# Optimization experiments

Hardware: AMD Instinct MI355X
Metric: run time of the kernel (lower is better)

The kernel has to match this reference:

```python
import jax, jax.numpy as jnp
import numpy as np

HIDDEN = 1024
HEADS = 16
HEAD_DIM = HIDDEN // HEADS

def setup_inputs() -> dict:
    key = jax.random.key(0)
    k1, k2, k3 = jax.random.split(key, 3)
    scale = 1.0 / np.sqrt(HIDDEN)
    return {
        "x": jax.random.normal(k1, (2, 2048, HIDDEN), dtype=jnp.float32),
        "w_qkv": jax.random.normal(k2, (HIDDEN, 3 * HIDDEN), dtype=jnp.float32) * scale,
        "b_qkv": jnp.zeros((3 * HIDDEN,), dtype=jnp.float32),
        "w_out": jax.random.normal(k3, (HIDDEN, HIDDEN), dtype=jnp.float32) * scale,
        "b_out": jnp.zeros((HIDDEN,), dtype=jnp.float32),
    }

def reference(x, w_qkv, b_qkv, w_out, b_out):
    B, S, H = x.shape
    qkv = x @ w_qkv + b_qkv                              # (B,S,3H)
    qkv = qkv.reshape(B, S, 3, HEADS, HEAD_DIM)
    qkv = jnp.transpose(qkv, (2, 0, 3, 1, 4))            # (3,B,nh,S,hd)
    q, k, v = qkv[0], qkv[1], qkv[2]
    scores = jnp.einsum("bhqd,bhkd->bhqk", q, k) / np.sqrt(HEAD_DIM)
    causal = jnp.triu(jnp.ones((S, S), dtype=bool), k=1)  # True above diagonal
    scores = jnp.where(causal, -jnp.inf, scores)
    attn = jax.nn.softmax(scores, axis=-1)               # dropout: eval mode (identity)
    out = jnp.einsum("bhqk,bhkd->bhqd", attn, v)
    out = jnp.transpose(out, (0, 2, 1, 3)).reshape(B, S, H)
    return out @ w_out + b_out
```

## Files before the change

### kernel.cpp

```cpp
#include <hip/hip_runtime.h>
#include <hip/hip_bf16.h>

typedef short short8 __attribute__((ext_vector_type(8)));
typedef float f32x4 __attribute__((ext_vector_type(4)));

typedef const __attribute__((address_space(1))) unsigned int* gas_ptr;
typedef __attribute__((address_space(3))) unsigned int* las_ptr;
#define ASYNC16(g, l) __builtin_amdgcn_global_load_lds((gas_ptr)(g), (las_ptr)(l), 16, 0, 0)

__device__ __forceinline__ unsigned short f2bf(float f) {
    unsigned int u = __builtin_bit_cast(unsigned int, f);
    u += 0x7fff + ((u >> 16) & 1);
    return (unsigned short)(u >> 16);
}
__device__ __forceinline__ float bf2f(unsigned short s) {
    unsigned int u = (unsigned int)s << 16;
    return __builtin_bit_cast(float, u);
}
__device__ __forceinline__ unsigned int pkbf_trunc(float lo, float hi) {
    return __builtin_amdgcn_perm(__builtin_bit_cast(unsigned int, hi),
                                 __builtin_bit_cast(unsigned int, lo), 0x07060302u);
}
__device__ __forceinline__ float fexp2(float x) {
#if __has_builtin(__builtin_amdgcn_exp2f)
    return __builtin_amdgcn_exp2f(x);
#else
    return __expf(x * 0.6931471805599453f);
#endif
}

__device__ __forceinline__ void transpose_tile(
    const float* __restrict__ w, unsigned short* __restrict__ wt,
    int K, int N, int k0, int n0, unsigned short* tile)
{
    for (int i = threadIdx.x; i < 64 * 64; i += 256) {
        int r = i >> 6, c = i & 63;
        tile[r * 65 + c] = f2bf(w[(size_t)(k0 + r) * N + n0 + c]);
    }
    __syncthreads();
    for (int i = threadIdx.x; i < 64 * 64; i += 256) {
        int r = i >> 6, c = i & 63;
        wt[(size_t)(n0 + r) * K + k0 + c] = tile[c * 65 + r];
    }
}

__global__ __launch_bounds__(256) void prep(
    const float* __restrict__ x, const float* __restrict__ w_qkv,
    const float* __restrict__ w_out,
    unsigned short* __restrict__ x_b, unsigned short* __restrict__ wqkv_t,
    unsigned short* __restrict__ wout_t)
{
    __shared__ unsigned short tile[64 * 65];
    int bid = blockIdx.x;
    if (bid < 4096) {
        int i = (bid * 256 + threadIdx.x) * 4;
        float4 v = *(const float4*)(x + i);
        ushort4 o;
        o.x = f2bf(v.x); o.y = f2bf(v.y); o.z = f2bf(v.z); o.w = f2bf(v.w);
        *(ushort4*)(x_b + i) = o;
    } else if (bid < 4096 + 768) {
        int t = bid - 4096;
        transpose_tile(w_qkv, wqkv_t, 1024, 3072, (t / 48) * 64, (t % 48) * 64, tile);
    } else {
        int t = bid - 4864;
        transpose_tile(w_out, wout_t, 1024, 1024, (t >> 4) * 64, (t & 15) * 64, tile);
    }
}


template<bool OUT_BF16, bool QKV>
__global__ __launch_bounds__(256, 3) void gemm_bt(
    const unsigned short* __restrict__ A,
    const unsigned short* __restrict__ Bt,
    const float* __restrict__ bias,
    void* __restrict__ C,
    unsigned short* __restrict__ vTp,
    int M, int N, int K)
{
    __shared__ __align__(16) unsigned short As[2][128 * 32];
    __shared__ __align__(16) unsigned short Bs[2][128 * 32];
    const int tid = threadIdx.x;
    const int lane = tid & 63;
    const int wave = tid >> 6;
    const int wr = wave >> 1, wc = wave & 1;
    const int m0 = blockIdx.x * 128, n0 = blockIdx.y * 128;
    const int fr = lane & 15, fq = lane >> 4;

    f32x4 acc[4][4] = {};

    const int grow = lane >> 2;
    const int gcol = (lane & 3) * 8;
    const unsigned short* Ag = A  + (size_t)(m0 + wave * 32 + grow) * K + gcol;
    const unsigned short* Bg = Bt + (size_t)(n0 + wave * 32 + grow) * K + gcol;
    const int wb0 = (wave * 32) * 32;
    const int wb1 = (wave * 32 + 16) * 32;

    for (int k0 = 0; k0 < K; k0 += 64) {
        __syncthreads();
        ASYNC16(Ag + k0,               As[0] + wb0);
        ASYNC16(Ag + 16 * K + k0,      As[0] + wb1);
        ASYNC16(Bg + k0,               Bs[0] + wb0);
        ASYNC16(Bg + 16 * K + k0,      Bs[0] + wb1);
        ASYNC16(Ag + k0 + 32,          As[1] + wb0);
        ASYNC16(Ag + 16 * K + k0 + 32, As[1] + wb1);
        ASYNC16(Bg + k0 + 32,          Bs[1] + wb0);
        ASYNC16(Bg + 16 * K + k0 + 32, Bs[1] + wb1);
        __syncthreads();

#pragma unroll
        for (int h = 0; h < 2; h++) {
            short8 af[4], bfr[4];
#pragma unroll
            for (int i = 0; i < 4; i++)
                af[i] = *(const short8*)(As[h] + (wr * 64 + i * 16 + fr) * 32 + fq * 8);
#pragma unroll
            for (int j = 0; j < 4; j++)
                bfr[j] = *(const short8*)(Bs[h] + (wc * 64 + j * 16 + fr) * 32 + fq * 8);
#pragma unroll
            for (int i = 0; i < 4; i++)
#pragma unroll
                for (int j = 0; j < 4; j++)
                    acc[i][j] = __builtin_amdgcn_mfma_f32_16x16x32_bf16(af[i], bfr[j], acc[i][j], 0, 0, 0);
        }
    }

#pragma unroll
    for (int i = 0; i < 4; i++)
#pragma unroll
        for (int j = 0; j < 4; j++) {
            int col = n0 + wc * 64 + j * 16 + fr;
            float bv = bias[col];
            if (QKV && col >= 2048) {
                int hh = (col - 2048) >> 6, d = col & 63;
#pragma unroll
                for (int r = 0; r < 4; r++) {
                    int row = m0 + wr * 64 + i * 16 + fq * 4 + r;
                    int bb = row >> 11, s = row & 2047;
                    vTp[((size_t)(bb * 16 + hh) * 64 + d) * 2048 + s] = f2bf(acc[i][j][r] + bv);
                }
            } else {
                const int cstride = QKV ? 2048 : N;
#pragma unroll
                for (int r = 0; r < 4; r++) {
                    int row = m0 + wr * 64 + i * 16 + fq * 4 + r;
                    float v = acc[i][j][r] + bv;
                    if (OUT_BF16)
                        ((unsigned short*)C)[(size_t)row * cstride + col] = f2bf(v);
                    else
                        ((float*)C)[(size_t)row * cstride + col] = v;
                }
            }
        }
}


template<int RG0>
__device__ __forceinline__ void attn_step(
    const unsigned short* __restrict__ Ks0, const unsigned short* __restrict__ Ks1,
    const unsigned short* __restrict__ Vs0, const unsigned short* __restrict__ Vs1,
    unsigned short* __restrict__ Psw,
    const short8 (&qf)[2][2], const short8 ones,
    f32x4 (&o_acc)[2][4], f32x4 (&l_acc)[2],
    int j0, int fr, int fq,
    const int (&qrow0)[2], bool diagA, bool diagB)
{
    const int kpos = ((fq + (fr >> 1)) & 3) * 8;
    short8 kf[4][2];
#pragma unroll
    for (int t = 0; t < 4; t++) {
        kf[t][0] = *(const short8*)(Ks0 + (t * 16 + fr) * 32 + kpos);
        kf[t][1] = *(const short8*)(Ks1 + (t * 16 + fr) * 32 + kpos);
    }

    const float C1 = 0.18033688011112042f;
    const float C2 = -11.541560327111707f;

#pragma unroll
    for (int rg = RG0; rg < 2; rg++) {
        f32x4 s[4];
        __builtin_amdgcn_s_setprio(1);
#pragma unroll
        for (int t = 0; t < 4; t++) {
            s[t] = (f32x4){0.f, 0.f, 0.f, 0.f};
            s[t] = __builtin_amdgcn_mfma_f32_16x16x32_bf16(kf[t][0], qf[rg][0], s[t], 0, 0, 0);
            s[t] = __builtin_amdgcn_mfma_f32_16x16x32_bf16(kf[t][1], qf[rg][1], s[t], 0, 0, 0);
        }
        __builtin_amdgcn_s_setprio(0);
        const bool diag = (rg == 0) ? diagA : diagB;
        unsigned short* prow = Psw + rg * (16 * 64);
        const int qr = qrow0[rg] + fr;
        if (diag) {
#pragma unroll
            for (int t = 0; t < 4; t++) {
                const int kb = j0 + t * 16 + fq * 4;
                float p[4];
#pragma unroll
                for (int r = 0; r < 4; r++) {
                    float v = fexp2(s[t][r] * C1 + C2);
                    if (kb + r > qr) v = 0.f;
                    p[r] = v;
                }
                uint2 pk;
                pk.x = pkbf_trunc(p[0], p[1]);
                pk.y = pkbf_trunc(p[2], p[3]);
                const int blk = (t * 2 + (fq >> 1) + fr) & 7;
                *(uint2*)(prow + fr * 64 + blk * 8 + (fq & 1) * 4) = pk;
            }
        } else {
#pragma unroll
            for (int t = 0; t < 4; t++) {
                float p[4];
#pragma unroll
                for (int r = 0; r < 4; r++)
                    p[r] = fexp2(s[t][r] * C1 + C2);
                uint2 pk;
                pk.x = pkbf_trunc(p[0], p[1]);
                pk.y = pkbf_trunc(p[2], p[3]);
                const int blk = (t * 2 + (fq >> 1) + fr) & 7;
                *(uint2*)(prow + fr * 64 + blk * 8 + (fq & 1) * 4) = pk;
            }
        }
    }

#pragma unroll
    for (int ks = 0; ks < 2; ks++) {
        const unsigned short* Vsb = ks ? Vs1 : Vs0;
        const int colp = ((ks * 4 + fq + fr) & 7) * 8;
        short8 pf[2];
#pragma unroll
        for (int rg = RG0; rg < 2; rg++)
            pf[rg] = *(const short8*)(Psw + rg * (16 * 64) + fr * 64 + colp);
        __builtin_amdgcn_s_setprio(1);
#pragma unroll
        for (int t = 0; t < 4; t++) {
            short8 vf = *(const short8*)(Vsb + (t * 16 + fr) * 32 + kpos);
#pragma unroll
            for (int rg = RG0; rg < 2; rg++)
                o_acc[rg][t] = __builtin_amdgcn_mfma_f32_16x16x32_bf16(pf[rg], vf, o_acc[rg][t], 0, 0, 0);
        }
#pragma unroll
        for (int rg = RG0; rg < 2; rg++)
            l_acc[rg] = __builtin_amdgcn_mfma_f32_16x16x32_bf16(pf[rg], ones, l_acc[rg], 0, 0, 0);
        __builtin_amdgcn_s_setprio(0);
    }
}

__global__ __launch_bounds__(256, 2) void flash_attn(
    const unsigned short* __restrict__ qkv,
    const unsigned short* __restrict__ vT,
    unsigned short* __restrict__ Opart,
    float* __restrict__ lpart)
{
    const int p = blockIdx.x;
    const int g = blockIdx.y;
    const int h = blockIdx.z & 15, b = blockIdx.z >> 4;
    const int tid = threadIdx.x, wave = tid >> 6, lane = tid & 63;
    const int fr = lane & 15, fq = lane >> 4;
    const size_t RS = 2048;

    const unsigned short* Qb = qkv + (size_t)b * 2048 * RS + h * 64;
    const unsigned short* Kb = Qb + 1024;
    const unsigned short* Vt = vT + (size_t)(b * 16 + h) * 64 * 2048;

    __shared__ __align__(16) unsigned short Ks[2][64 * 32];
    __shared__ __align__(16) unsigned short Vs[2][64 * 32];
    __shared__ __align__(16) unsigned short Ps[4][2 * 16 * 64];

    short8 qf[2][2];
    int qrow0[2];
#pragma unroll
    for (int rg = 0; rg < 2; rg++) {
        int qt = (rg == 0) ? p : (31 - p);
        qrow0[rg] = qt * 64 + wave * 16;
        const unsigned short* qrow = Qb + (size_t)(qrow0[rg] + fr) * RS;
        qf[rg][0] = *(const short8*)(qrow + fq * 8);
        qf[rg][1] = *(const short8*)(qrow + 32 + fq * 8);
    }
    short8 ones;
#pragma unroll
    for (int e = 0; e < 8; e++) ones[e] = (short)0x3F80;

    f32x4 o_acc[2][4] = {};
    f32x4 l_acc[2] = {};

    const int grow = lane >> 2;
    const int gswz = (((lane & 3) - (grow >> 1)) & 3) * 8;
    const unsigned short* Kg = Kb + (size_t)(wave * 16 + grow) * RS + gswz;
    const unsigned short* Vg = Vt + (size_t)(wave * 16 + grow) * 2048 + gswz;
    const int wb = wave * 16 * 32;

    const int mid = (p >= 8) ? 8 : (16 - p);
    const int lo = g ? mid : 0;
    const int hi = g ? (32 - p) : mid;

    for (int jt = lo; jt < hi; jt++) {
        const int j0 = jt * 64;
        __syncthreads();
        ASYNC16(Kg + (size_t)j0 * RS,       Ks[0] + wb);
        ASYNC16(Kg + (size_t)j0 * RS + 32,  Ks[1] + wb);
        ASYNC16(Vg + j0,                    Vs[0] + wb);
        ASYNC16(Vg + j0 + 32,               Vs[1] + wb);
        __syncthreads();

        bool diagA = (jt == p), diagB = (jt == 31 - p);
        if (jt <= p)
            attn_step<0>(Ks[0], Ks[1], Vs[0], Vs[1], Ps[wave], qf, ones,
                         o_acc, l_acc, j0, fr, fq, qrow0, diagA, diagB);
        else
            attn_step<1>(Ks[0], Ks[1], Vs[0], Vs[1], Ps[wave], qf, ones,
                         o_acc, l_acc, j0, fr, fq, qrow0, diagA, diagB);
    }

    unsigned short* Og = Opart + (size_t)g * 4096 * 1024;
    float* lg = lpart + (size_t)g * 4096 * 16;
#pragma unroll
    for (int rg = 0; rg < 2; rg++) {
#pragma unroll
        for (int t = 0; t < 4; t++)
#pragma unroll
            for (int r = 0; r < 4; r++) {
                int row = qrow0[rg] + fq * 4 + r;
                Og[(size_t)(b * 2048 + row) * 1024 + h * 64 + t * 16 + fr] = f2bf(o_acc[rg][t][r]);
            }
        if (fr == 0) {
#pragma unroll
            for (int r = 0; r < 4; r++) {
                int row = qrow0[rg] + fq * 4 + r;
                lg[(size_t)(b * 2048 + row) * 16 + h] = l_acc[rg][r];
            }
        }
    }
}

__global__ __launch_bounds__(256) void reduce_attn(
    const unsigned short* __restrict__ Opart, const float* __restrict__ lpart,
    unsigned short* __restrict__ out)
{
    int i = (blockIdx.x * 256 + threadIdx.x) * 8;
    int row = i >> 10, h = (i & 1023) >> 6;
    float lsum = lpart[(size_t)row * 16 + h] + lpart[(size_t)4096 * 16 + row * 16 + h];
    float inv = 1.0f / lsum;
    ushort4 a0 = *(const ushort4*)(Opart + i);
    ushort4 a1 = *(const ushort4*)(Opart + i + 4);
    ushort4 b0 = *(const ushort4*)(Opart + (size_t)4096 * 1024 + i);
    ushort4 b1 = *(const ushort4*)(Opart + (size_t)4096 * 1024 + i + 4);
    ushort4 o0, o1;
    o0.x = f2bf((bf2f(a0.x) + bf2f(b0.x)) * inv);
    o0.y = f2bf((bf2f(a0.y) + bf2f(b0.y)) * inv);
    o0.z = f2bf((bf2f(a0.z) + bf2f(b0.z)) * inv);
    o0.w = f2bf((bf2f(a0.w) + bf2f(b0.w)) * inv);
    o1.x = f2bf((bf2f(a1.x) + bf2f(b1.x)) * inv);
    o1.y = f2bf((bf2f(a1.y) + bf2f(b1.y)) * inv);
    o1.z = f2bf((bf2f(a1.z) + bf2f(b1.z)) * inv);
    o1.w = f2bf((bf2f(a1.w) + bf2f(b1.w)) * inv);
    *(ushort4*)(out + i) = o0;
    *(ushort4*)(out + i + 4) = o1;
}

extern "C" void kernel_launch(void* const* d_in, const int* in_sizes, int n_in,
                              void* d_out, int out_size, void* d_ws, size_t ws_size,
                              hipStream_t stream) {
    const float* x      = (const float*)d_in[0];
    const float* w_qkv  = (const float*)d_in[1];
    const float* b_qkv  = (const float*)d_in[2];
    const float* w_out  = (const float*)d_in[3];
    const float* b_out  = (const float*)d_in[4];
    float* out = (float*)d_out;

    char* ws = (char*)d_ws;
    unsigned short* x_b    = (unsigned short*)(ws);
    unsigned short* wqkv_t = (unsigned short*)(ws + 8u  * 1024 * 1024);
    unsigned short* wout_t = (unsigned short*)(ws + 14u * 1024 * 1024);
    unsigned short* qkv    = (unsigned short*)(ws + 16u * 1024 * 1024);
    unsigned short* attn   = (unsigned short*)(ws + 32u * 1024 * 1024);
    unsigned short* vT     = (unsigned short*)(ws + 40u * 1024 * 1024);
    unsigned short* Opart  = (unsigned short*)(ws + 48u * 1024 * 1024);
    float*          lpart  = (float*)         (ws + 64u * 1024 * 1024);

    prep<<<5120, 256, 0, stream>>>(x, w_qkv, w_out, x_b, wqkv_t, wout_t);
    gemm_bt<true, true ><<<dim3(32, 24), 256, 0, stream>>>(x_b,  wqkv_t, b_qkv, qkv, vT, 4096, 3072, 1024);
    flash_attn<<<dim3(16, 2, 32), 256, 0, stream>>>(qkv, vT, Opart, lpart);
    reduce_attn<<<2048, 256, 0, stream>>>(Opart, lpart, attn);
    gemm_bt<false, false><<<dim3(32, 8),  256, 0, stream>>>(attn, wout_t, b_out, out, nullptr, 4096, 1024, 1024);
}
```

Baseline: 189.1 us.

## Prefetch next K/V tile into registers during attention compute

Replaces the synchronous global_load_lds K/V tile loads with register prefetching. The next tile is loaded into registers while the current tile is computed, then written to LDS between barriers. This is meant to hide global memory latency behind the MFMA work, at the cost of extra VGPRs and an explicit LDS store step.

```diff
diff --git a/kernel.cpp b/kernel.cpp
--- a/kernel.cpp
+++ b/kernel.cpp
@@ -3,6 +3,7 @@
 
 typedef short short8 __attribute__((ext_vector_type(8)));
 typedef float f32x4 __attribute__((ext_vector_type(4)));
+typedef unsigned int uint4v __attribute__((ext_vector_type(4)));
 
 typedef const __attribute__((address_space(1))) unsigned int* gas_ptr;
 typedef __attribute__((address_space(3))) unsigned int* las_ptr;
@@ -289,18 +290,37 @@
     const unsigned short* Vg = Vt + (size_t)(wave * 16 + grow) * 2048 + gswz;
     const int wb = wave * 16 * 32;
 
+    unsigned short* dK0 = Ks[0] + wb + lane * 8;
+    unsigned short* dK1 = Ks[1] + wb + lane * 8;
+    unsigned short* dV0 = Vs[0] + wb + lane * 8;
+    unsigned short* dV1 = Vs[1] + wb + lane * 8;
+
     const int mid = (p >= 8) ? 8 : (16 - p);
     const int lo = g ? mid : 0;
     const int hi = g ? (32 - p) : mid;
 
+    {
+        const int j0 = lo * 64;
+        uint4v aK0 = *(const uint4v*)(Kg + (size_t)j0 * RS);
+        uint4v aK1 = *(const uint4v*)(Kg + (size_t)j0 * RS + 32);
+        uint4v aV0 = *(const uint4v*)(Vg + j0);
+        uint4v aV1 = *(const uint4v*)(Vg + j0 + 32);
+        *(uint4v*)dK0 = aK0;
+        *(uint4v*)dK1 = aK1;
+        *(uint4v*)dV0 = aV0;
+        *(uint4v*)dV1 = aV1;
+    }
+    __syncthreads();
+
     for (int jt = lo; jt < hi; jt++) {
         const int j0 = jt * 64;
-        __syncthreads();
-        ASYNC16(Kg + (size_t)j0 * RS,       Ks[0] + wb);
-        ASYNC16(Kg + (size_t)j0 * RS + 32,  Ks[1] + wb);
-        ASYNC16(Vg + j0,                    Vs[0] + wb);
-        ASYNC16(Vg + j0 + 32,               Vs[1] + wb);
-        __syncthreads();
+        const bool more = (jt + 1 < hi);
+        const int j0n = more ? (j0 + 64) : j0;
+
+        uint4v aK0 = *(const uint4v*)(Kg + (size_t)j0n * RS);
+        uint4v aK1 = *(const uint4v*)(Kg + (size_t)j0n * RS + 32);
+        uint4v aV0 = *(const uint4v*)(Vg + j0n);
+        uint4v aV1 = *(const uint4v*)(Vg + j0n + 32);
 
         bool diagA = (jt == p), diagB = (jt == 31 - p);
         if (jt <= p)
@@ -309,6 +329,15 @@
         else
             attn_step<1>(Ks[0], Ks[1], Vs[0], Vs[1], Ps[wave], qf, ones,
                          o_acc, l_acc, j0, fr, fq, qrow0, diagA, diagB);
+
+        __syncthreads();
+        if (more) {
+            *(uint4v*)dK0 = aK0;
+            *(uint4v*)dK1 = aK1;
+            *(uint4v*)dV0 = aV0;
+            *(uint4v*)dV1 = aV1;
+        }
+        __syncthreads();
     }
 
     unsigned short* Og = Opart + (size_t)g * 4096 * 1024;
```

Result: no change. 187.4 us (-0.9%).
